# Performance work log

Hardware: AMD Instinct MI355X
Metric: run time of the kernel (lower is better)

Reference implementation:

```python
import jax, jax.numpy as jnp
import numpy as np

KERNEL = 4  # conv kernel_size == stride


def setup_inputs() -> dict:
    key = jax.random.key(0)
    k1, k2, k3, k4 = jax.random.split(key, 4)
    x = jax.random.normal(k1, (16, 3, 512, 512), dtype=jnp.float32)
    w_sample = jax.random.normal(k2, (64, 3, KERNEL, KERNEL), dtype=jnp.float32) * 0.1
    b_sample = jax.random.normal(k3, (64,), dtype=jnp.float32) * 0.1
    centers = jax.random.uniform(k4, (8,), dtype=jnp.float32)
    return {"x": x, "w_sample": w_sample, "b_sample": b_sample, "centers": centers}


def _spectral_normalize(w):
    # torch spectral_norm divides the weight by its top singular value
    # (estimated by power iteration; we compute it exactly, same math at convergence)
    wm = w.reshape(w.shape[0], -1)  # [out, in*kh*kw]
    sigma = jnp.linalg.svd(wm, compute_uv=False)[0]
    return w / sigma


def _forward(x, w_sample, b_sample, centers):
    wn = _spectral_normalize(w_sample)
    # strided conv: 3 -> C channels, kernel=stride=4, no padding  -> [B,C,H/4,W/4]
    y = jax.lax.conv_general_dilated(
        x, wn, window_strides=(KERNEL, KERNEL), padding='VALID',
        dimension_numbers=('NCHW', 'OIHW', 'NCHW'))
    y = y + b_sample[None, :, None, None]
    # soft VQ: squared distance to each center, softmax(-dist)-weighted sum of centers
    quant_dist = (y[..., None] - centers) ** 2          # [B,C,H',W',K]
    soft = jnp.sum(centers * jax.nn.softmax(-quant_dist, axis=-1), axis=-1)
    return soft


def reference(x, w_sample, b_sample, centers):
    return _forward(x, w_sample, b_sample, centers)
```

## Files before the change

kernel.cpp:

```cpp
#include <hip/hip_runtime.h>
#include <stdint.h>

#define CIN 3
#define WW 512
#define HW (512 * 512)
#define COUT 64
#define KF 48
#define HO 128
#define WO 128
#define LDA 52

#define NTAB 2048
#define YMIN (-12.0f)
#define YMAX (12.0f)
#define INVH ((float)NTAB / (YMAX - YMIN))
#define WS_TAB_OFF 128
#define WS_WP_HI 4352
#define WS_WP_LO 5888
#define WS_FLOATS (WS_WP_LO + 1536)

typedef __attribute__((ext_vector_type(8))) short short8;
typedef __attribute__((ext_vector_type(16))) float f32x16;

union FragU { uint32_t u[4]; short8 s; };

__device__ __forceinline__ uint32_t pack_bf16_pair(float f0, float f1) {
  return (__float_as_uint(f0) >> 16) | (__float_as_uint(f1) & 0xffff0000u);
}
__device__ __forceinline__ float trunc_bf16f(float f) {
  return __uint_as_float(__float_as_uint(f) & 0xffff0000u);
}
__device__ __forceinline__ void split_pair(float4 a, float4 b, short8& hi, short8& lo) {
  FragU h, l;
  h.u[0] = pack_bf16_pair(a.x, a.y);
  h.u[1] = pack_bf16_pair(a.z, a.w);
  h.u[2] = pack_bf16_pair(b.x, b.y);
  h.u[3] = pack_bf16_pair(b.z, b.w);
  l.u[0] = pack_bf16_pair(a.x - trunc_bf16f(a.x), a.y - trunc_bf16f(a.y));
  l.u[1] = pack_bf16_pair(a.z - trunc_bf16f(a.z), a.w - trunc_bf16f(a.w));
  l.u[2] = pack_bf16_pair(b.x - trunc_bf16f(b.x), b.y - trunc_bf16f(b.y));
  l.u[3] = pack_bf16_pair(b.z - trunc_bf16f(b.z), b.w - trunc_bf16f(b.w));
  hi = h.s; lo = l.s;
}

__device__ __forceinline__ float vq_eval(float y, const float* __restrict__ c) {
  float d[8], m;
#pragma unroll
  for (int k = 0; k < 8; ++k) { float t = y - c[k]; d[k] = t * t; }
  m = fminf(fminf(fminf(d[0], d[1]), fminf(d[2], d[3])),
            fminf(fminf(d[4], d[5]), fminf(d[6], d[7])));
  float num = 0.f, den = 0.f;
#pragma unroll
  for (int k = 0; k < 8; ++k) {
    float e = __expf(m - d[k]);
    den += e;
    num = fmaf(c[k], e, num);
  }
  return num / den;
}

__global__ __launch_bounds__(256) void prep_sigma(
    const float* __restrict__ w, const float* __restrict__ bias,
    const float* __restrict__ centers, float* __restrict__ ws, int build_tab) {
  const int t = threadIdx.x;

  if (blockIdx.x == 1) {
    float c[8];
#pragma unroll
    for (int k = 0; k < 8; ++k) c[k] = centers[k];
    const float h = (YMAX - YMIN) / (float)NTAB;
#pragma unroll 1
    for (int k = t; k < NTAB; k += 256) {
      float y0 = YMIN + (float)k * h;
      float f0 = vq_eval(y0, c);
      float f1 = vq_eval(y0 + h, c);
      ws[WS_TAB_OFF + 2 * k]     = f0;
      ws[WS_TAB_OFF + 2 * k + 1] = f1 - f0;
    }
    if (t < COUT) ws[2 + t] = (bias[t] - YMIN) * INVH;
    return;
  }

  __shared__ float sW[COUT * KF];
  __shared__ float sG[KF * LDA];
  __shared__ float sA[KF * LDA];
  __shared__ float sB[KF * LDA];
  __shared__ float sv[64];
  __shared__ float sp[256];
  __shared__ float s_a;

  {
    const float4* w4 = (const float4*)w;
    float4* s4 = (float4*)sW;
#pragma unroll
    for (int q = 0; q < 3; ++q) s4[q * 256 + t] = w4[q * 256 + t];
  }
  __syncthreads();

  const int ti = t >> 4, tj = t & 15;
  const int i0 = 3 * ti, j0 = 3 * tj;
  {
    float acc[3][3] = {{0.f}};
#pragma unroll 4
    for (int m = 0; m < COUT; ++m) {
      const float* wr = sW + m * KF;
      float a0 = wr[i0], a1 = wr[i0 + 1], a2 = wr[i0 + 2];
      float b0 = wr[j0], b1 = wr[j0 + 1], b2 = wr[j0 + 2];
      acc[0][0] = fmaf(a0, b0, acc[0][0]);
      acc[0][1] = fmaf(a0, b1, acc[0][1]);
      acc[0][2] = fmaf(a0, b2, acc[0][2]);
      acc[1][0] = fmaf(a1, b0, acc[1][0]);
      acc[1][1] = fmaf(a1, b1, acc[1][1]);
      acc[1][2] = fmaf(a1, b2, acc[1][2]);
      acc[2][0] = fmaf(a2, b0, acc[2][0]);
      acc[2][1] = fmaf(a2, b1, acc[2][1]);
      acc[2][2] = fmaf(a2, b2, acc[2][2]);
    }
#pragma unroll
    for (int ii = 0; ii < 3; ++ii)
#pragma unroll
      for (int jj = 0; jj < 3; ++jj) {
        sG[(i0 + ii) * LDA + j0 + jj] = acc[ii][jj];
        sA[(i0 + ii) * LDA + j0 + jj] = acc[ii][jj];
      }
  }
  __syncthreads();

#pragma unroll 1
  for (int s = 0; s < 4; ++s) {
    const float* src = (s & 1) ? sB : sA;
    float* dst = (s & 1) ? sA : sB;
    float acc[3][3] = {{0.f}};
#pragma unroll
    for (int q = 0; q < 12; ++q) {
      float4 ar0 = *(const float4*)(src + (i0 + 0) * LDA + 4 * q);
      float4 ar1 = *(const float4*)(src + (i0 + 1) * LDA + 4 * q);
      float4 ar2 = *(const float4*)(src + (i0 + 2) * LDA + 4 * q);
      float4 br0 = *(const float4*)(src + (j0 + 0) * LDA + 4 * q);
      float4 br1 = *(const float4*)(src + (j0 + 1) * LDA + 4 * q);
      float4 br2 = *(const float4*)(src + (j0 + 2) * LDA + 4 * q);
#define DOT4(A, B, C) \
      C = fmaf(A.x, B.x, C); C = fmaf(A.y, B.y, C); \
      C = fmaf(A.z, B.z, C); C = fmaf(A.w, B.w, C);
      DOT4(ar0, br0, acc[0][0]); DOT4(ar0, br1, acc[0][1]); DOT4(ar0, br2, acc[0][2]);
      DOT4(ar1, br0, acc[1][0]); DOT4(ar1, br1, acc[1][1]); DOT4(ar1, br2, acc[1][2]);
      DOT4(ar2, br0, acc[2][0]); DOT4(ar2, br1, acc[2][1]); DOT4(ar2, br2, acc[2][2]);
#undef DOT4
    }
    __syncthreads();
#pragma unroll
    for (int ii = 0; ii < 3; ++ii)
#pragma unroll
      for (int jj = 0; jj < 3; ++jj)
        dst[(i0 + ii) * LDA + j0 + jj] = acc[ii][jj];
    __syncthreads();
  }
  const float* M = sA;

  if (t < 64) sv[t] = (t < KF) ? 1.0f : 0.f;
  __syncthreads();

#pragma unroll 1
  for (int it = 0; it < 6; ++it) {
    float partial = 0.f;
    if (t < 192) {
      const int row = t >> 2, seg = t & 3;
      const float* mr = M + row * LDA + seg * 12;
      const float4* v4 = (const float4*)sv;
#pragma unroll
      for (int q = 0; q < 3; ++q) {
        float4 m4 = *(const float4*)(mr + 4 * q);
        float4 vv = v4[seg * 3 + q];
        partial = fmaf(m4.x, vv.x, partial);
        partial = fmaf(m4.y, vv.y, partial);
        partial = fmaf(m4.z, vv.z, partial);
        partial = fmaf(m4.w, vv.w, partial);
      }
    }
    sp[t] = partial;
    __syncthreads();
    if (t < 64) {
      float nv = 0.f;
      if (t < KF) nv = (sp[4 * t] + sp[4 * t + 1]) + (sp[4 * t + 2] + sp[4 * t + 3]);
      float ss = nv * nv;
#pragma unroll
      for (int m = 32; m >= 1; m >>= 1) ss += __shfl_xor(ss, m, 64);
      sv[t] = (t < KF) ? nv * rsqrtf(ss) : 0.f;
    }
    __syncthreads();
  }

  {
    float partial = 0.f;
    if (t < 192) {
      const int row = t >> 2, seg = t & 3;
      const float* mr = sG + row * LDA + seg * 12;
      const float4* v4 = (const float4*)sv;
#pragma unroll
      for (int q = 0; q < 3; ++q) {
        float4 m4 = *(const float4*)(mr + 4 * q);
        float4 vv = v4[seg * 3 + q];
        partial = fmaf(m4.x, vv.x, partial);
        partial = fmaf(m4.y, vv.y, partial);
        partial = fmaf(m4.z, vv.z, partial);
        partial = fmaf(m4.w, vv.w, partial);
      }
    }
    sp[t] = partial;
    __syncthreads();
    if (t < 64) {
      float nv = 0.f;
      if (t < KF) nv = (sp[4 * t] + sp[4 * t + 1]) + (sp[4 * t + 2] + sp[4 * t + 3]);
      float vt = sv[t];
      float num = nv * vt;
      float den = vt * vt;
#pragma unroll
      for (int m = 32; m >= 1; m >>= 1) {
        num += __shfl_xor(num, m, 64);
        den += __shfl_xor(den, m, 64);
      }
      if (t == 0) {
        float sg = sqrtf(num / den);
        ws[0] = sg;
        ws[1] = INVH / sg;
        s_a = INVH / sg;
      }
    }
  }
  __syncthreads();

  if (build_tab) {
    const float a = s_a;
#pragma unroll 1
    for (int slot = t; slot < 384; slot += 256) {
      const int ct = slot / 192;
      const int rm = slot % 192;
      const int kk = rm >> 6;
      const int l  = rm & 63;
      const int row = ct * 32 + (l & 31);
      const int kbase = kk * 16 + (l >> 5) * 8;
      const float* src = w + row * KF + kbase;
      float4 fa = *(const float4*)(src);
      float4 fb = *(const float4*)(src + 4);
      fa.x *= a; fa.y *= a; fa.z *= a; fa.w *= a;
      fb.x *= a; fb.y *= a; fb.z *= a; fb.w *= a;
      short8 hi, lo;
      split_pair(fa, fb, hi, lo);
      *(short8*)(ws + WS_WP_HI + slot * 4) = hi;
      *(short8*)(ws + WS_WP_LO + slot * 4) = lo;
    }
  }
}

__global__ __launch_bounds__(256) void conv_vq_mfma2(
    const float* __restrict__ x, const float* __restrict__ params,
    float* __restrict__ out) {
  __shared__ float stab[2 * NTAB];
  __shared__ float sso[COUT];
  const int t = threadIdx.x;
  {
    const float4* src = (const float4*)(params + WS_TAB_OFF);
    float4* dst = (float4*)stab;
#pragma unroll
    for (int q = 0; q < 4; ++q) dst[q * 256 + t] = src[q * 256 + t];
    if (t < COUT) sso[t] = params[2 + t];
  }
  __syncthreads();

  const int lane = t & 63;
  const int wv   = t >> 6;
  const int ct   = wv & 1;
  const int pt   = wv >> 1;
  const int h    = lane >> 5;
  const int pl   = lane & 31;

  const int n0   = blockIdx.x * 64;
  const int b    = n0 >> 14;
  const int rem0 = n0 & 16383;
  const int i    = rem0 >> 7;
  const int jj   = (rem0 & 127) + pt * 32 + pl;

  const float* xb = x + (size_t)b * (CIN * HW) + (size_t)(4 * i) * WW + 4 * jj;
  float4 xf[3][2];
#pragma unroll
  for (int kk = 0; kk < 3; ++kk) {
    xf[kk][0] = *(const float4*)(xb + (size_t)kk * HW + (2 * h) * WW);
    xf[kk][1] = *(const float4*)(xb + (size_t)kk * HW + (2 * h + 1) * WW);
  }
  short8 Bh[3], Bl[3];
#pragma unroll
  for (int kk = 0; kk < 3; ++kk) split_pair(xf[kk][0], xf[kk][1], Bh[kk], Bl[kk]);

  const short8* AhP = (const short8*)(params + WS_WP_HI) + ct * 192 + lane;
  const short8* AlP = (const short8*)(params + WS_WP_LO) + ct * 192 + lane;
  short8 Ah[3], Al[3];
#pragma unroll
  for (int kk = 0; kk < 3; ++kk) { Ah[kk] = AhP[kk * 64]; Al[kk] = AlP[kk * 64]; }

  f32x16 acc;
  {
    const float* sob = sso + ct * 32 + 4 * h;
#pragma unroll
    for (int r = 0; r < 16; ++r) acc[r] = sob[(r & 3) + 8 * (r >> 2)];
  }

#pragma unroll
  for (int kk = 0; kk < 3; ++kk)
    acc = __builtin_amdgcn_mfma_f32_32x32x16_bf16(Ah[kk], Bh[kk], acc, 0, 0, 0);
#pragma unroll
  for (int kk = 0; kk < 3; ++kk) {
    acc = __builtin_amdgcn_mfma_f32_32x32x16_bf16(Ah[kk], Bl[kk], acc, 0, 0, 0);
    acc = __builtin_amdgcn_mfma_f32_32x32x16_bf16(Al[kk], Bh[kk], acc, 0, 0, 0);
  }

  const float2* tab2 = (const float2*)stab;
  float* ob = out + ((size_t)(b * COUT + ct * 32 + 4 * h)) * 16384 + i * 128 + jj;
#pragma unroll
  for (int r = 0; r < 16; ++r) {
    float u = acc[r];
    u = fmaxf(u, 0.0f);
    u = fminf(u, (float)NTAB - 0.0005f);
    const int k = (int)u;
    const float fr = u - (float)k;
    const float2 e = tab2[k];
    ob[(size_t)((r & 3) + 8 * (r >> 2)) * 16384] = fmaf(fr, e.y, e.x);
  }
}

__global__ __launch_bounds__(256) void conv_vq_exp(
    const float* __restrict__ x, const float* __restrict__ w,
    const float* __restrict__ bias, const float* __restrict__ centers,
    const float* __restrict__ sigma_ptr, float* __restrict__ out) {
  const int t = threadIdx.x;
  const int pos = blockIdx.x * 256 + t;
  const int b   = pos >> 14;
  const int rem = pos & 16383;
  const int i   = rem >> 7;
  const int j   = rem & 127;

  const float inv_sigma = 1.0f / sigma_ptr[0];
  float cc[8], tc[8], mc2[8];
#pragma unroll
  for (int k = 0; k < 8; ++k) {
    float c = centers[k];
    cc[k] = c; tc[k] = 2.0f * c; mc2[k] = -c * c;
  }
  const float* xp = x + (size_t)b * (CIN * HW) + (size_t)(4 * i) * WW + 4 * j;
  float p[KF];
#pragma unroll
  for (int ci = 0; ci < CIN; ++ci)
#pragma unroll
    for (int kh = 0; kh < 4; ++kh) {
      float4 v4 = *(const float4*)(xp + (size_t)ci * HW + kh * WW);
      p[(ci * 4 + kh) * 4 + 0] = v4.x;
      p[(ci * 4 + kh) * 4 + 1] = v4.y;
      p[(ci * 4 + kh) * 4 + 2] = v4.z;
      p[(ci * 4 + kh) * 4 + 3] = v4.w;
    }
  float* op = out + (size_t)b * (COUT * HO * WO) + rem;
#pragma unroll 2
  for (int c = 0; c < COUT; ++c) {
    const float4* wr = (const float4*)(w + c * KF);
    float a0 = 0.f, a1 = 0.f, a2 = 0.f, a3 = 0.f;
#pragma unroll
    for (int q = 0; q < 12; ++q) {
      float4 gq = wr[q];
      a0 = fmaf(p[4*q+0], gq.x, a0);
      a1 = fmaf(p[4*q+1], gq.y, a1);
      a2 = fmaf(p[4*q+2], gq.z, a2);
      a3 = fmaf(p[4*q+3], gq.w, a3);
    }
    const float y = fmaf((a0 + a1) + (a2 + a3), inv_sigma, bias[c]);
    float e0 = __expf(fmaf(tc[0], y, mc2[0])), e1 = __expf(fmaf(tc[1], y, mc2[1]));
    float e2 = __expf(fmaf(tc[2], y, mc2[2])), e3 = __expf(fmaf(tc[3], y, mc2[3]));
    float e4 = __expf(fmaf(tc[4], y, mc2[4])), e5 = __expf(fmaf(tc[5], y, mc2[5]));
    float e6 = __expf(fmaf(tc[6], y, mc2[6])), e7 = __expf(fmaf(tc[7], y, mc2[7]));
    float den = ((e0 + e1) + (e2 + e3)) + ((e4 + e5) + (e6 + e7));
    float num = (fmaf(cc[0], e0, cc[1] * e1) + fmaf(cc[2], e2, cc[3] * e3)) +
                (fmaf(cc[4], e4, cc[5] * e5) + fmaf(cc[6], e6, cc[7] * e7));
    op[(size_t)c * (HO * WO)] = __fdividef(num, den);
  }
}

extern "C" void kernel_launch(void* const* d_in, const int* in_sizes, int n_in,
                              void* d_out, int out_size, void* d_ws, size_t ws_size,
                              hipStream_t stream) {
  const float* x       = (const float*)d_in[0];
  const float* w       = (const float*)d_in[1];
  const float* b       = (const float*)d_in[2];
  const float* centers = (const float*)d_in[3];
  float* out = (float*)d_out;
  float* ws  = (float*)d_ws;

  const int use_table = (ws_size >= (size_t)WS_FLOATS * sizeof(float)) ? 1 : 0;

  prep_sigma<<<use_table ? 2 : 1, 256, 0, stream>>>(w, b, centers, ws, use_table);
  if (use_table)
    conv_vq_mfma2<<<(16 * HO * WO) / 64, 256, 0, stream>>>(x, ws, out);
  else
    conv_vq_exp<<<(16 * HO * WO) / 256, 256, 0, stream>>>(x, w, b, centers, ws, out);
}
```

Measured before the change: 39.44 us.

## Replace split-bf16 triple MFMA with single fp16 MFMA and vectorized output stores

Swaps the hi/lo bf16 split (9 MFMAs per tile) for a single fp16 conversion of inputs and pre-scaled weights, using 3 f16 MFMAs. It also swaps the A/B operands so each lane holds one channel and consecutive pixels, allowing float4 output stores instead of scalar strided stores. Fewer conversion ALU ops, less weight traffic, and wider writes are the intended savings. The risk is lower accuracy from fp16 round-toward-zero on the inputs, and possible fp16 range issues.

After: 41.15 us. 1.04x slower.

```diff
diff --git a/kernel.cpp b/kernel.cpp
--- a/kernel.cpp
+++ b/kernel.cpp
@@ -15,32 +15,22 @@
 #define YMAX (12.0f)
 #define INVH ((float)NTAB / (YMAX - YMIN))
 #define WS_TAB_OFF 128
-#define WS_WP_HI 4352
-#define WS_WP_LO 5888
-#define WS_FLOATS (WS_WP_LO + 1536)
-
-typedef __attribute__((ext_vector_type(8))) short short8;
+#define WS_WP 4224
+#define WS_FLOATS (WS_WP + 1536)
+
 typedef __attribute__((ext_vector_type(16))) float f32x16;
-
-union FragU { uint32_t u[4]; short8 s; };
-
-__device__ __forceinline__ uint32_t pack_bf16_pair(float f0, float f1) {
-  return (__float_as_uint(f0) >> 16) | (__float_as_uint(f1) & 0xffff0000u);
-}
-__device__ __forceinline__ float trunc_bf16f(float f) {
-  return __uint_as_float(__float_as_uint(f) & 0xffff0000u);
-}
-__device__ __forceinline__ void split_pair(float4 a, float4 b, short8& hi, short8& lo) {
-  FragU h, l;
-  h.u[0] = pack_bf16_pair(a.x, a.y);
-  h.u[1] = pack_bf16_pair(a.z, a.w);
-  h.u[2] = pack_bf16_pair(b.x, b.y);
-  h.u[3] = pack_bf16_pair(b.z, b.w);
-  l.u[0] = pack_bf16_pair(a.x - trunc_bf16f(a.x), a.y - trunc_bf16f(a.y));
-  l.u[1] = pack_bf16_pair(a.z - trunc_bf16f(a.z), a.w - trunc_bf16f(a.w));
-  l.u[2] = pack_bf16_pair(b.x - trunc_bf16f(b.x), b.y - trunc_bf16f(b.y));
-  l.u[3] = pack_bf16_pair(b.z - trunc_bf16f(b.z), b.w - trunc_bf16f(b.w));
-  hi = h.s; lo = l.s;
+typedef __fp16 half2t __attribute__((ext_vector_type(2)));
+typedef __fp16 half8 __attribute__((ext_vector_type(8)));
+
+union H8 { half8 h; half2t h2[4]; __fp16 e[8]; uint32_t u[4]; float f[4]; };
+
+__device__ __forceinline__ half8 cvt8_rtz(float4 a, float4 b) {
+  H8 r;
+  r.h2[0] = __builtin_amdgcn_cvt_pkrtz(a.x, a.y);
+  r.h2[1] = __builtin_amdgcn_cvt_pkrtz(a.z, a.w);
+  r.h2[2] = __builtin_amdgcn_cvt_pkrtz(b.x, b.y);
+  r.h2[3] = __builtin_amdgcn_cvt_pkrtz(b.z, b.w);
+  return r.h;
 }
 
 __device__ __forceinline__ float vq_eval(float y, const float* __restrict__ c) {
@@ -232,27 +222,32 @@
   if (build_tab) {
     const float a = s_a;
 #pragma unroll 1
-    for (int slot = t; slot < 384; slot += 256) {
-      const int ct = slot / 192;
-      const int rm = slot % 192;
-      const int kk = rm >> 6;
-      const int l  = rm & 63;
-      const int row = ct * 32 + (l & 31);
+    for (int sl = t; sl < 384; sl += 256) {
+      const int grp = sl >> 6;
+      const int ct = grp / 3;
+      const int kk = grp % 3;
+      const int l  = sl & 63;
+      const int ch = ct * 32 + (l & 31);
       const int kbase = kk * 16 + (l >> 5) * 8;
-      const float* src = w + row * KF + kbase;
+      const float* src = w + ch * KF + kbase;
       float4 fa = *(const float4*)(src);
       float4 fb = *(const float4*)(src + 4);
-      fa.x *= a; fa.y *= a; fa.z *= a; fa.w *= a;
-      fb.x *= a; fb.y *= a; fb.z *= a; fb.w *= a;
-      short8 hi, lo;
-      split_pair(fa, fb, hi, lo);
-      *(short8*)(ws + WS_WP_HI + slot * 4) = hi;
-      *(short8*)(ws + WS_WP_LO + slot * 4) = lo;
-    }
-  }
-}
-
-__global__ __launch_bounds__(256) void conv_vq_mfma2(
+      H8 r;
+      r.e[0] = (__fp16)(fa.x * a);
+      r.e[1] = (__fp16)(fa.y * a);
+      r.e[2] = (__fp16)(fa.z * a);
+      r.e[3] = (__fp16)(fa.w * a);
+      r.e[4] = (__fp16)(fb.x * a);
+      r.e[5] = (__fp16)(fb.y * a);
+      r.e[6] = (__fp16)(fb.z * a);
+      r.e[7] = (__fp16)(fb.w * a);
+      *(float4*)(ws + WS_WP + sl * 4) =
+          make_float4(r.f[0], r.f[1], r.f[2], r.f[3]);
+    }
+  }
+}
+
+__global__ __launch_bounds__(256) void conv_vq_mfma3(
     const float* __restrict__ x, const float* __restrict__ params,
     float* __restrict__ out) {
   __shared__ float stab[2 * NTAB];
@@ -281,49 +276,48 @@
   const int jj   = (rem0 & 127) + pt * 32 + pl;
 
   const float* xb = x + (size_t)b * (CIN * HW) + (size_t)(4 * i) * WW + 4 * jj;
-  float4 xf[3][2];
+  half8 Xf[3];
 #pragma unroll
   for (int kk = 0; kk < 3; ++kk) {
-    xf[kk][0] = *(const float4*)(xb + (size_t)kk * HW + (2 * h) * WW);
-    xf[kk][1] = *(const float4*)(xb + (size_t)kk * HW + (2 * h + 1) * WW);
-  }
-  short8 Bh[3], Bl[3];
-#pragma unroll
-  for (int kk = 0; kk < 3; ++kk) split_pair(xf[kk][0], xf[kk][1], Bh[kk], Bl[kk]);
-
-  const short8* AhP = (const short8*)(params + WS_WP_HI) + ct * 192 + lane;
-  const short8* AlP = (const short8*)(params + WS_WP_LO) + ct * 192 + lane;
-  short8 Ah[3], Al[3];
-#pragma unroll
-  for (int kk = 0; kk < 3; ++kk) { Ah[kk] = AhP[kk * 64]; Al[kk] = AlP[kk * 64]; }
-
+    float4 fa = *(const float4*)(xb + (size_t)kk * HW + (2 * h) * WW);
+    float4 fb = *(const float4*)(xb + (size_t)kk * HW + (2 * h + 1) * WW);
+    Xf[kk] = cvt8_rtz(fa, fb);
+  }
+
+  const half8* wp = (const half8*)(params + WS_WP);
+  half8 Wf[3];
+#pragma unroll
+  for (int kk = 0; kk < 3; ++kk) Wf[kk] = wp[(ct * 3 + kk) * 64 + lane];
+
+  const int ch = ct * 32 + pl;
+  const float och = sso[ch];
   f32x16 acc;
-  {
-    const float* sob = sso + ct * 32 + 4 * h;
-#pragma unroll
-    for (int r = 0; r < 16; ++r) acc[r] = sob[(r & 3) + 8 * (r >> 2)];
-  }
+#pragma unroll
+  for (int r = 0; r < 16; ++r) acc[r] = och;
 
 #pragma unroll
   for (int kk = 0; kk < 3; ++kk)
-    acc = __builtin_amdgcn_mfma_f32_32x32x16_bf16(Ah[kk], Bh[kk], acc, 0, 0, 0);
-#pragma unroll
-  for (int kk = 0; kk < 3; ++kk) {
-    acc = __builtin_amdgcn_mfma_f32_32x32x16_bf16(Ah[kk], Bl[kk], acc, 0, 0, 0);
-    acc = __builtin_amdgcn_mfma_f32_32x32x16_bf16(Al[kk], Bh[kk], acc, 0, 0, 0);
-  }
+    acc = __builtin_amdgcn_mfma_f32_32x32x16_f16(Xf[kk], Wf[kk], acc, 0, 0, 0);
 
   const float2* tab2 = (const float2*)stab;
-  float* ob = out + ((size_t)(b * COUT + ct * 32 + 4 * h)) * 16384 + i * 128 + jj;
-#pragma unroll
-  for (int r = 0; r < 16; ++r) {
-    float u = acc[r];
-    u = fmaxf(u, 0.0f);
-    u = fminf(u, (float)NTAB - 0.0005f);
-    const int k = (int)u;
-    const float fr = u - (float)k;
-    const float2 e = tab2[k];
-    ob[(size_t)((r & 3) + 8 * (r >> 2)) * 16384] = fmaf(fr, e.y, e.x);
+  float* ob = out + ((size_t)(b * COUT + ch)) * 16384 + i * 128 +
+              (rem0 & 127) + pt * 32 + 4 * h;
+#pragma unroll
+  for (int q = 0; q < 4; ++q) {
+    float4 res;
+#pragma unroll
+    for (int m = 0; m < 4; ++m) {
+      float u = acc[4 * q + m];
+      u = fmaxf(u, 0.0f);
+      u = fminf(u, (float)NTAB - 0.0005f);
+      const int k = (int)u;
+      const float fr = u - (float)k;
+      const float2 e = tab2[k];
+      float v = fmaf(fr, e.y, e.x);
+      if (m == 0) res.x = v; else if (m == 1) res.y = v;
+      else if (m == 2) res.z = v; else res.w = v;
+    }
+    *(float4*)(ob + 8 * q) = res;
   }
 }
 
@@ -396,7 +390,7 @@
 
   prep_sigma<<<use_table ? 2 : 1, 256, 0, stream>>>(w, b, centers, ws, use_table);
   if (use_table)
-    conv_vq_mfma2<<<(16 * HO * WO) / 64, 256, 0, stream>>>(x, ws, out);
+    conv_vq_mfma3<<<(16 * HO * WO) / 64, 256, 0, stream>>>(x, ws, out);
   else
     conv_vq_exp<<<(16 * HO * WO) / 256, 256, 0, stream>>>(x, w, b, centers, ws, out);
 }
```
